# Kernel tuning notes

Measured on AMD Instinct MI355X. Metric: run time of the kernel, lower is better.

The kernel has to match this reference:

```python
import jax, jax.numpy as jnp
import numpy as np

B, T, E = 2, 4096, 768
H = 12
WIN = 256  # one-sided window w; band width = 2w+1


def setup_inputs() -> dict:
    key = jax.random.key(0)
    k1, k2, k3, k4 = jax.random.split(key, 4)
    scale = 1.0 / np.sqrt(E)
    return {
        "x": jax.random.normal(k1, (B, T, E), dtype=jnp.float32),
        "Wq": jax.random.normal(k2, (E, E), dtype=jnp.float32) * scale,
        "Wk": jax.random.normal(k3, (E, E), dtype=jnp.float32) * scale,
        "Wv": jax.random.normal(k4, (E, E), dtype=jnp.float32) * scale,
    }


def reference(x, Wq, Wk, Wv):
    b, t, e = x.shape
    h, w = H, WIN
    s = e // h
    Wb = 2 * w + 1          # band width
    nc = t // w             # number of query chunks of size w

    # projections (nn.Linear, bias=False): y = x @ W^T
    q = (x @ Wq.T).reshape(b, t, h, s) * (1.0 / np.sqrt(s))
    k = (x @ Wk.T).reshape(b, t, h, s)
    v = (x @ Wv.T).reshape(b, t, h, s)

    # overlapping key/value chunks: chunk c covers absolute keys [c*w - w, c*w + 2w)
    pad = [(0, 0), (w, w), (0, 0), (0, 0)]
    kp = jnp.pad(k, pad).reshape(b, nc + 2, w, h, s)
    k3 = jnp.concatenate([kp[:, :-2], kp[:, 1:-1], kp[:, 2:]], axis=2)  # [b,nc,3w,h,s]
    vp = jnp.pad(v, pad).reshape(b, nc + 2, w, h, s)
    v3 = jnp.concatenate([vp[:, :-2], vp[:, 1:-1], vp[:, 2:]], axis=2)  # [b,nc,3w,h,s]

    qc = q.reshape(b, nc, w, h, s)
    scores = jnp.einsum('bcxhd,bcyhd->bhcxy', qc, k3)  # [b,h,nc,w,3w]

    # extract the banded diagonals: band j <-> key index p + j in the 3w window
    idx = jnp.arange(w)[:, None] + jnp.arange(Wb)[None, :]  # [w, 2w+1], values in [0,3w)
    band = jnp.take_along_axis(scores, idx[None, None, None], axis=-1)  # [b,h,nc,w,2w+1]
    band = band.reshape(b, h, t, Wb).transpose(0, 2, 1, 3)  # [b,t,h,2w+1]

    # mask_invalid_locations: key absolute pos = i + j - w must lie in [0, t)
    key_pos = jnp.arange(t)[:, None] + jnp.arange(Wb)[None, :] - w
    invalid = (key_pos < 0) | (key_pos >= t)
    band = jnp.where(invalid[None, :, None, :], -jnp.inf, band)

    probs = jax.nn.softmax(band.astype(jnp.float32), axis=-1).astype(x.dtype)

    # sliding_chunks_matmul_pv: scatter band probs back to the 3w window layout
    pc = probs.transpose(0, 2, 1, 3).reshape(b, h, nc, w, Wb)
    pc_pad = jnp.pad(pc, [(0, 0)] * 4 + [(w - 1, w - 1)])  # last axis len 4w-1
    # full[p, m] = band[p, m - p] for m-p in [0, 2w], else 0
    idx2 = (jnp.arange(3 * w)[None, :] - jnp.arange(w)[:, None]) + (w - 1)  # [w, 3w]
    pfull = jnp.take_along_axis(pc_pad, idx2[None, None, None], axis=-1)  # [b,h,nc,w,3w]

    out = jnp.einsum('bhcpm,bcmhd->bcphd', pfull, v3).reshape(b, t, e)
    return out
```

## Files before the change

kernel.cpp:

```cpp
#include <hip/hip_runtime.h>

#define B_ 2
#define T_ 4096
#define E_ 768
#define H_ 12
#define S_ 64
#define WIN_ 256
#define GX_ 32
#define TP_ 4128

typedef unsigned short u16;
typedef unsigned int u32;
typedef __attribute__((ext_vector_type(8))) short bf16x8;
typedef __attribute__((ext_vector_type(4))) short bf16x4;
typedef __attribute__((ext_vector_type(4))) float f32x4;

__device__ __forceinline__ u16 f2bf(float f) {
  u32 u = __float_as_uint(f);
  u += ((u >> 16) & 1u) + 0x7fffu;
  return (u16)(u >> 16);
}

__device__ __forceinline__ u32 cvt_pk_bf16(float lo, float hi) {
  u32 r;
  asm("v_cvt_pk_bf16_f32 %0, %1, %2" : "=v"(r) : "v"(lo), "v"(hi));
  return r;
}

__device__ __forceinline__ void async_copy16(const u16* g, u16* l) {
  __builtin_amdgcn_global_load_lds(
      (const __attribute__((address_space(1))) void*)g,
      (__attribute__((address_space(3))) void*)l, 16, 0, 0);
}

__global__ void cvt_all(const float* __restrict__ x, const float* __restrict__ wq,
                        const float* __restrict__ wk, const float* __restrict__ wv,
                        u16* __restrict__ xb, u16* __restrict__ wb) {
  const int n4x = B_ * T_ * E_ / 4;
  const int n4w = E_ * E_ / 4;
  int i = blockIdx.x * 256 + threadIdx.x;
  const float* src;
  u16* dst;
  int j;
  if (i < n4x) {
    src = x; dst = xb; j = i;
  } else {
    int t = i - n4x;
    int z = t / n4w;
    if (z >= 3) return;
    j = t - z * n4w;
    src = (z == 0) ? wq : ((z == 1) ? wk : wv);
    dst = wb + (size_t)z * E_ * E_;
  }
  float4 v = ((const float4*)src)[j];
  ushort4 o;
  o.x = f2bf(v.x); o.y = f2bf(v.y); o.z = f2bf(v.z); o.w = f2bf(v.w);
  ((ushort4*)dst)[j] = o;
}

__global__ __launch_bounds__(256)
void gemm_qkv(const u16* __restrict__ xb, const u16* __restrict__ wb,
              u16* __restrict__ qkv) {
  const int M = B_ * T_;
  __shared__ u16 As[2][128][64];
  __shared__ u16 Bs[2][128][64];
  int tid = threadIdx.x;
  int lane = tid & 63, wave = tid >> 6;
  int wr = wave >> 1, wc = wave & 1;
  int q8 = lane >> 4, nl = lane & 15;
  int bm = blockIdx.x * 128, bn = blockIdx.y * 128;
  int z = blockIdx.z;
  const u16* A = xb;
  const u16* Bmat = wb + (size_t)z * E_ * E_;
  u16* C = qkv + (size_t)z * M * E_;
  float scale = (z == 0) ? (0.125f * 1.44269504088896f) : 1.0f;

  int r0 = tid >> 3, c0 = tid & 7;
  int cs = c0 ^ (r0 & 7);
  const u16* ga = A + (size_t)(bm + r0) * E_ + cs * 8;
  const u16* gb = Bmat + (size_t)(bn + r0) * E_ + cs * 8;
  int ld = tid * 8;

  int sw0 = (q8 ^ (nl & 7)) * 8;

  const int NK = E_ / 64;
#pragma unroll
  for (int m = 0; m < 4; ++m) {
    async_copy16(ga + (size_t)(32 * m) * E_, &As[0][0][0] + ld + m * 2048);
    async_copy16(gb + (size_t)(32 * m) * E_, &Bs[0][0][0] + ld + m * 2048);
  }

  f32x4 acc[4][4] = {};

#define KSTEP(KI, BUF, NBUF)                                                   \
  {                                                                            \
    asm volatile("s_waitcnt lgkmcnt(0)" ::: "memory");                         \
    __builtin_amdgcn_s_barrier();                                              \
    __builtin_amdgcn_sched_barrier(0);                                         \
    int kp = ((KI) + 1 < NK) ? (KI) + 1 : NK - 1;                              \
    int koff = kp * 64;                                                        \
    _Pragma("unroll")                                                          \
    for (int m = 0; m < 4; ++m) {                                              \
      async_copy16(ga + (size_t)(32 * m) * E_ + koff,                          \
                   &As[NBUF][0][0] + ld + m * 2048);                           \
      async_copy16(gb + (size_t)(32 * m) * E_ + koff,                          \
                   &Bs[NBUF][0][0] + ld + m * 2048);                           \
    }                                                                          \
    asm volatile("s_waitcnt vmcnt(8) lgkmcnt(0)" ::: "memory");                \
    __builtin_amdgcn_sched_barrier(0);                                         \
    _Pragma("unroll")                                                          \
    for (int kk = 0; kk < 2; ++kk) {                                           \
      bf16x8 af[4], bfr[4];                                                    \
      int sw = sw0 ^ (kk * 32);                                                \
      _Pragma("unroll")                                                        \
      for (int i = 0; i < 4; ++i)                                              \
        af[i] = *(const bf16x8*)&As[BUF][wr * 64 + i * 16 + nl][sw];           \
      _Pragma("unroll")                                                        \
      for (int i = 0; i < 4; ++i)                                              \
        bfr[i] = *(const bf16x8*)&Bs[BUF][wc * 64 + i * 16 + nl][sw];          \
      __builtin_amdgcn_s_setprio(1);                                           \
      _Pragma("unroll")                                                        \
      for (int i = 0; i < 4; ++i)                                              \
        _Pragma("unroll")                                                      \
        for (int j2 = 0; j2 < 4; ++j2)                                         \
          acc[i][j2] = __builtin_amdgcn_mfma_f32_16x16x32_bf16(af[i], bfr[j2], \
                                                               acc[i][j2], 0, 0, 0); \
      __builtin_amdgcn_s_setprio(0);                                           \
    }                                                                          \
  }

  for (int kb = 0; kb < NK; kb += 2) {
    KSTEP(kb + 0, 0, 1)
    KSTEP(kb + 1, 1, 0)
  }
#undef KSTEP

#pragma unroll
  for (int i = 0; i < 4; ++i)
#pragma unroll
    for (int j2 = 0; j2 < 4; ++j2)
#pragma unroll
      for (int r = 0; r < 4; ++r) {
        int row = bm + wr * 64 + i * 16 + q8 * 4 + r;
        int col = bn + wc * 64 + j2 * 16 + nl;
        C[(size_t)row * E_ + col] = f2bf(acc[i][j2][r] * scale);
      }
}

__global__ void transpose_v(const u16* __restrict__ v, u16* __restrict__ vT) {
  __shared__ u16 lt[64][66];
  int t = threadIdx.x;
  int t0 = blockIdx.x * 64;
  int e0 = blockIdx.y * 64;
  int b = blockIdx.z;
#pragma unroll
  for (int i = 0; i < 2; ++i) {
    int u = t + i * 256;
    int tok = u >> 3, cg = u & 7;
    bf16x8 val = *(const bf16x8*)(v + (size_t)(b * T_ + t0 + tok) * E_ + e0 + cg * 8);
#pragma unroll
    for (int j = 0; j < 8; ++j) lt[tok][cg * 8 + j] = (u16)val[j];
  }
  __syncthreads();
#pragma unroll
  for (int i = 0; i < 2; ++i) {
    int u = t + i * 256;
    int d = u >> 3, ck = u & 7;
    bf16x8 o;
#pragma unroll
    for (int j = 0; j < 8; ++j) o[j] = (short)lt[ck * 8 + j][d];
    *(bf16x8*)(vT + (size_t)(b * E_ + e0 + d) * TP_ + t0 + ck * 8) = o;
  }
}

__global__ __launch_bounds__(256)
void attn_kernel(const u16* __restrict__ qkv, const u16* __restrict__ vT,
                 float* __restrict__ out) {
  const int Mtot = B_ * T_;
  const u16* qb = qkv;
  const u16* kb = qkv + (size_t)Mtot * E_;

  int tid = threadIdx.x;
  int lane = tid & 63, wave = tid >> 6;
  int q8 = lane >> 4, nl = lane & 15;

  int d = blockIdx.y * GX_ + blockIdx.x;
  int xcd = d & 7, jj = d >> 3;
  int nx = xcd * 4 + (jj & 3);
  int ny = jj >> 2;
  int qs = nx * 128;
  int b = ny / H_, h = ny % H_;
  int qw = qs + wave * 32;
  size_t ho = (size_t)h * S_;

  bf16x8 aq[2][2];
#pragma unroll
  for (int mt = 0; mt < 2; ++mt) {
    const u16* qrow = qb + (size_t)(b * T_ + qw + mt * 16 + nl) * E_ + ho;
    aq[mt][0] = *(const bf16x8*)(qrow + q8 * 8);
    aq[mt][1] = *(const bf16x8*)(qrow + 32 + q8 * 8);
  }

  f32x4 O[2][4] = {};
  float lacc[2] = {0.f, 0.f};

  int klo = qw - WIN_; if (klo < 0) klo = 0;
  int khi = qw + 32 + WIN_; if (khi > T_) khi = T_;

  const u16* kbase = kb + (size_t)b * T_ * E_ + ho;
  const u16* vbase = vT + ((size_t)b * E_ + ho) * TP_;

  int alo = ((((q8 << 1) & 3) << 4) + nl) << 2;
  int ahi = alo + 64;
  bool hint = q8 >= 2;

  bf16x8 bk[2][2];
#pragma unroll
  for (int nt = 0; nt < 2; ++nt) {
    const u16* krow = kbase + (size_t)(klo + nt * 16 + nl) * E_;
    bk[nt][0] = *(const bf16x8*)(krow + q8 * 8);
    bk[nt][1] = *(const bf16x8*)(krow + 32 + q8 * 8);
  }

  for (int kt = klo; kt < khi; kt += 32) {
    bf16x8 bv[4];
#pragma unroll
    for (int dt = 0; dt < 4; ++dt)
      bv[dt] = *(const bf16x8*)(vbase + (size_t)(dt * 16 + nl) * TP_ + kt + q8 * 8);

    int ktn = (kt + 32 < khi) ? kt + 32 : kt;
    bf16x8 nbk[2][2];
#pragma unroll
    for (int nt = 0; nt < 2; ++nt) {
      const u16* krow = kbase + (size_t)(ktn + nt * 16 + nl) * E_;
      nbk[nt][0] = *(const bf16x8*)(krow + q8 * 8);
      nbk[nt][1] = *(const bf16x8*)(krow + 32 + q8 * 8);
    }

    f32x4 sc[2][2] = {};
    __builtin_amdgcn_s_setprio(1);
#pragma unroll
    for (int nt = 0; nt < 2; ++nt)
#pragma unroll
      for (int mt = 0; mt < 2; ++mt) {
        sc[mt][nt] = __builtin_amdgcn_mfma_f32_16x16x32_bf16(bk[nt][0], aq[mt][0], sc[mt][nt], 0, 0, 0);
        sc[mt][nt] = __builtin_amdgcn_mfma_f32_16x16x32_bf16(bk[nt][1], aq[mt][1], sc[mt][nt], 0, 0, 0);
      }
    __builtin_amdgcn_s_setprio(0);

    if (kt < qw - 225 || kt > qw + 225) {
#pragma unroll
      for (int mt = 0; mt < 2; ++mt)
#pragma unroll
        for (int nt = 0; nt < 2; ++nt)
#pragma unroll
          for (int r = 0; r < 4; ++r) {
            int qa = qw + mt * 16 + nl;
            int ka = kt + nt * 16 + q8 * 4 + r;
            int dd = ka - qa;
            sc[mt][nt][r] = (dd < -WIN_ || dd > WIN_) ? -1e30f : sc[mt][nt][r];
          }
    }

#pragma unroll
    for (int mt = 0; mt < 2; ++mt) {
      float s = 0.f;
#pragma unroll
      for (int nt = 0; nt < 2; ++nt)
#pragma unroll
        for (int r = 0; r < 4; ++r) {
          float p = exp2f(sc[mt][nt][r]);
          sc[mt][nt][r] = p;
          s += p;
        }
      lacc[mt] += s;
    }

    bf16x8 ap[2];
#pragma unroll
    for (int mt = 0; mt < 2; ++mt) {
      u32 pk00 = cvt_pk_bf16(sc[mt][0][0], sc[mt][0][1]);
      u32 pk01 = cvt_pk_bf16(sc[mt][0][2], sc[mt][0][3]);
      u32 pk10 = cvt_pk_bf16(sc[mt][1][0], sc[mt][1][1]);
      u32 pk11 = cvt_pk_bf16(sc[mt][1][2], sc[mt][1][3]);
      int q0a = __builtin_amdgcn_ds_bpermute(alo, (int)pk00);
      int q0b = __builtin_amdgcn_ds_bpermute(alo, (int)pk10);
      int q1a = __builtin_amdgcn_ds_bpermute(alo, (int)pk01);
      int q1b = __builtin_amdgcn_ds_bpermute(alo, (int)pk11);
      int q2a = __builtin_amdgcn_ds_bpermute(ahi, (int)pk00);
      int q2b = __builtin_amdgcn_ds_bpermute(ahi, (int)pk10);
      int q3a = __builtin_amdgcn_ds_bpermute(ahi, (int)pk01);
      int q3b = __builtin_amdgcn_ds_bpermute(ahi, (int)pk11);
      union { u32 w[4]; bf16x8 v; } u;
      u.w[0] = (u32)(hint ? q0b : q0a);
      u.w[1] = (u32)(hint ? q1b : q1a);
      u.w[2] = (u32)(hint ? q2b : q2a);
      u.w[3] = (u32)(hint ? q3b : q3a);
      ap[mt] = u.v;
    }

    __builtin_amdgcn_s_setprio(1);
#pragma unroll
    for (int dt = 0; dt < 4; ++dt)
#pragma unroll
      for (int mt = 0; mt < 2; ++mt)
        O[mt][dt] = __builtin_amdgcn_mfma_f32_16x16x32_bf16(ap[mt], bv[dt], O[mt][dt], 0, 0, 0);
    __builtin_amdgcn_s_setprio(0);

#pragma unroll
    for (int nt = 0; nt < 2; ++nt) {
      bk[nt][0] = nbk[nt][0];
      bk[nt][1] = nbk[nt][1];
    }
  }

#pragma unroll
  for (int mt = 0; mt < 2; ++mt) {
    lacc[mt] += __shfl_xor(lacc[mt], 16);
    lacc[mt] += __shfl_xor(lacc[mt], 32);
  }

#pragma unroll
  for (int mt = 0; mt < 2; ++mt)
#pragma unroll
    for (int r = 0; r < 4; ++r) {
      float lq = __shfl(lacc[mt], (lane & 48) | (q8 * 4 + r));
      float inv = 1.0f / lq;
      int qa = qw + mt * 16 + q8 * 4 + r;
      float* op = out + (size_t)(b * T_ + qa) * E_ + ho;
#pragma unroll
      for (int dt = 0; dt < 4; ++dt)
        op[dt * 16 + nl] = O[mt][dt][r] * inv;
    }
}

extern "C" void kernel_launch(void* const* d_in, const int* in_sizes, int n_in,
                              void* d_out, int out_size, void* d_ws, size_t ws_size,
                              hipStream_t stream) {
  const float* x  = (const float*)d_in[0];
  const float* Wq = (const float*)d_in[1];
  const float* Wk = (const float*)d_in[2];
  const float* Wv = (const float*)d_in[3];
  float* out = (float*)d_out;

  const size_t M = (size_t)B_ * T_;
  u16* xb  = (u16*)d_ws;
  u16* wb  = xb + M * E_;
  u16* qkv = wb + 3 * (size_t)E_ * E_;
  u16* vT  = xb;

  const int n4x = B_ * T_ * E_ / 4;
  const int n4w = E_ * E_ / 4;
  int cvt_blocks = (n4x + 3 * n4w + 255) / 256;
  cvt_all<<<cvt_blocks, 256, 0, stream>>>(x, Wq, Wk, Wv, xb, wb);

  dim3 g1(M / 128, E_ / 128, 3);
  gemm_qkv<<<g1, 256, 0, stream>>>(xb, wb, qkv);

  dim3 gt(T_ / 64, E_ / 64, B_);
  transpose_v<<<gt, 256, 0, stream>>>(qkv + 2 * M * E_, vT);

  dim3 g2(GX_, B_ * H_);
  attn_kernel<<<g2, 256, 0, stream>>>(qkv, vT, out);
}
```

Before: 177.6 us.

## Split key range across wave pairs in attention kernel and merge via LDS

Each block now handles 64 queries instead of 128. Two waves share the same 32 queries and take alternating 32-key tiles. The partial O and row-sum accumulators from the odd wave are written to shared memory and added into the even wave's accumulators before normalization and store. This doubles the grid and halves the serial key loop per wave, with the aim of more parallelism and better latency hiding. The cost is an LDS reduction, a block barrier, and duplicate Q loads. The merge works because the softmax appears to use no running max, so partial sums can be added directly.

```diff
diff --git a/kernel.cpp b/kernel.cpp
--- a/kernel.cpp
+++ b/kernel.cpp
@@ -6,7 +6,7 @@
 #define H_ 12
 #define S_ 64
 #define WIN_ 256
-#define GX_ 32
+#define GXA_ 64
 #define TP_ 4128
 
 typedef unsigned short u16;
@@ -180,17 +180,21 @@
   const u16* qb = qkv;
   const u16* kb = qkv + (size_t)Mtot * E_;
 
+  __shared__ float cb[2][64][35];
+
   int tid = threadIdx.x;
   int lane = tid & 63, wave = tid >> 6;
+  int pair = wave >> 1;
+  int phase = wave & 1;
   int q8 = lane >> 4, nl = lane & 15;
 
-  int d = blockIdx.y * GX_ + blockIdx.x;
+  int d = blockIdx.y * GXA_ + blockIdx.x;
   int xcd = d & 7, jj = d >> 3;
-  int nx = xcd * 4 + (jj & 3);
-  int ny = jj >> 2;
-  int qs = nx * 128;
+  int nx = xcd * 8 + (jj & 7);
+  int ny = jj >> 3;
+  int qs = nx * 64;
   int b = ny / H_, h = ny % H_;
-  int qw = qs + wave * 32;
+  int qw = qs + pair * 32;
   size_t ho = (size_t)h * S_;
 
   bf16x8 aq[2][2];
@@ -206,6 +210,7 @@
 
   int klo = qw - WIN_; if (klo < 0) klo = 0;
   int khi = qw + 32 + WIN_; if (khi > T_) khi = T_;
+  int kst = klo + phase * 32;
 
   const u16* kbase = kb + (size_t)b * T_ * E_ + ho;
   const u16* vbase = vT + ((size_t)b * E_ + ho) * TP_;
@@ -217,18 +222,18 @@
   bf16x8 bk[2][2];
 #pragma unroll
   for (int nt = 0; nt < 2; ++nt) {
-    const u16* krow = kbase + (size_t)(klo + nt * 16 + nl) * E_;
+    const u16* krow = kbase + (size_t)(kst + nt * 16 + nl) * E_;
     bk[nt][0] = *(const bf16x8*)(krow + q8 * 8);
     bk[nt][1] = *(const bf16x8*)(krow + 32 + q8 * 8);
   }
 
-  for (int kt = klo; kt < khi; kt += 32) {
+  for (int kt = kst; kt < khi; kt += 64) {
     bf16x8 bv[4];
 #pragma unroll
     for (int dt = 0; dt < 4; ++dt)
       bv[dt] = *(const bf16x8*)(vbase + (size_t)(dt * 16 + nl) * TP_ + kt + q8 * 8);
 
-    int ktn = (kt + 32 < khi) ? kt + 32 : kt;
+    int ktn = (kt + 64 < khi) ? kt + 64 : kt;
     bf16x8 nbk[2][2];
 #pragma unroll
     for (int nt = 0; nt < 2; ++nt) {
@@ -314,24 +319,48 @@
     }
   }
 
-#pragma unroll
-  for (int mt = 0; mt < 2; ++mt) {
-    lacc[mt] += __shfl_xor(lacc[mt], 16);
-    lacc[mt] += __shfl_xor(lacc[mt], 32);
-  }
-
-#pragma unroll
-  for (int mt = 0; mt < 2; ++mt)
-#pragma unroll
-    for (int r = 0; r < 4; ++r) {
-      float lq = __shfl(lacc[mt], (lane & 48) | (q8 * 4 + r));
-      float inv = 1.0f / lq;
-      int qa = qw + mt * 16 + q8 * 4 + r;
-      float* op = out + (size_t)(b * T_ + qa) * E_ + ho;
+  if (phase == 1) {
+    float* dst = &cb[pair][lane][0];
+#pragma unroll
+    for (int mt = 0; mt < 2; ++mt)
 #pragma unroll
       for (int dt = 0; dt < 4; ++dt)
-        op[dt * 16 + nl] = O[mt][dt][r] * inv;
-    }
+#pragma unroll
+        for (int r = 0; r < 4; ++r) dst[mt * 16 + dt * 4 + r] = O[mt][dt][r];
+    dst[32] = lacc[0];
+    dst[33] = lacc[1];
+  }
+  __syncthreads();
+  if (phase == 0) {
+    const float* src = &cb[pair][lane][0];
+#pragma unroll
+    for (int mt = 0; mt < 2; ++mt)
+#pragma unroll
+      for (int dt = 0; dt < 4; ++dt)
+#pragma unroll
+        for (int r = 0; r < 4; ++r) O[mt][dt][r] += src[mt * 16 + dt * 4 + r];
+    lacc[0] += src[32];
+    lacc[1] += src[33];
+
+#pragma unroll
+    for (int mt = 0; mt < 2; ++mt) {
+      lacc[mt] += __shfl_xor(lacc[mt], 16);
+      lacc[mt] += __shfl_xor(lacc[mt], 32);
+    }
+
+#pragma unroll
+    for (int mt = 0; mt < 2; ++mt)
+#pragma unroll
+      for (int r = 0; r < 4; ++r) {
+        float lq = __shfl(lacc[mt], (lane & 48) | (q8 * 4 + r));
+        float inv = 1.0f / lq;
+        int qa = qw + mt * 16 + q8 * 4 + r;
+        float* op = out + (size_t)(b * T_ + qa) * E_ + ho;
+#pragma unroll
+        for (int dt = 0; dt < 4; ++dt)
+          op[dt * 16 + nl] = O[mt][dt][r] * inv;
+      }
+  }
 }
 
 extern "C" void kernel_launch(void* const* d_in, const int* in_sizes, int n_in,
@@ -360,6 +389,6 @@
   dim3 gt(T_ / 64, E_ / 64, B_);
   transpose_v<<<gt, 256, 0, stream>>>(qkv + 2 * M * E_, vT);
 
-  dim3 g2(GX_, B_ * H_);
+  dim3 g2(GXA_, B_ * H_);
   attn_kernel<<<g2, 256, 0, stream>>>(qkv, vT, out);
 }
```

After: 177.9 us. About the same (+0.2%).
